# Performance work log

Hardware: AMD Instinct MI355X
Metric: run time of the kernel (lower is better)

Reference implementation:

```python
import jax, jax.numpy as jnp
import numpy as np

B, T, N, D = 8, 512, 64, 128
PRED, HEADS, HID = 96, 8, 256
KERNELS = (17, 49)
NUM_LAYERS = 1
NUM_BLOCKS = 1
IDX_T = np.arange(64)   # lowest 64 of T//2=256 rfft modes (mode_select='low')
IDX_C = np.arange(32)   # min(modes, (N+1)//2)=32 lowest channel-frequency modes


def _mov_avg(x, k):
    # x: [B, T, N]; replicate-pad (k-1)//2 on both ends, then box filter (AvgPool1d stride 1)
    pad = (k - 1) // 2
    xp = jnp.concatenate([jnp.repeat(x[:, :1], pad, axis=1), x, jnp.repeat(x[:, -1:], pad, axis=1)], axis=1)
    c = jnp.cumsum(xp, axis=1)
    c = jnp.concatenate([jnp.zeros_like(c[:, :1]), c], axis=1)
    return (c[:, k:] - c[:, :-k]) / k


def _decomp_multi(x, dec_w, dec_b):
    # series_decomp_multi: softmax-weighted mixture of moving averages
    mm = jnp.stack([_mov_avg(x, k) for k in KERNELS], axis=-1)        # [B,T,N,K]
    w = jax.nn.softmax(x[..., None] * dec_w + dec_b, axis=-1)         # Linear(1,K) on x, softmax over K
    trend = jnp.sum(mm * w, axis=-1)
    return x - trend, trend


def _complex_attn(x, Wq, Wk, Wv, Wo):
    # x: complex64 [B, L, M, D]; multi-head attention over the M selected frequency modes.
    # Real projection weights applied to complex activations; attention weights are
    # softmax over |q k^H| / sqrt(dh); values stay complex.
    Bq, L, M, Dm = x.shape
    dh = Dm // HEADS
    q = jnp.einsum('blmd,de->blme', x, Wq).reshape(Bq, L, M, HEADS, dh)
    k = jnp.einsum('blmd,de->blme', x, Wk).reshape(Bq, L, M, HEADS, dh)
    v = jnp.einsum('blmd,de->blme', x, Wv).reshape(Bq, L, M, HEADS, dh)
    s = jnp.einsum('blmhd,blnhd->blhmn', q, jnp.conj(k))              # complex scores
    w = jax.nn.softmax(jnp.abs(s) / np.sqrt(dh), axis=-1)             # real attn weights
    o = jnp.einsum('blhmn,blnhd->blmhd', w.astype(x.dtype), v).reshape(Bq, L, M, Dm)
    return jnp.einsum('blmd,de->blme', o, Wo)


def _cem(x, Wq, Wk, Wv, Wo):
    # channel-frequency attention; x: [B, N, T, D]
    xp = jnp.transpose(x, (0, 2, 1, 3))                               # [B,T,N,D]
    xf = jnp.fft.rfft(xp, axis=2)                                     # [B,T,N//2+1,D]
    xs = xf[:, :, IDX_C, :]                                           # gather selected modes
    for _ in range(NUM_LAYERS):
        xs = _complex_attn(xs, Wq, Wk, Wv, Wo)
    yf = jnp.zeros((x.shape[0], T, N // 2 + 1, D), dtype=xf.dtype).at[:, :, IDX_C, :].set(xs)
    y = jnp.fft.irfft(yf, n=N, axis=2)
    return jnp.transpose(y, (0, 2, 1, 3))


def _tem(x, Wq, Wk, Wv, Wo):
    # temporal-frequency attention; x: [B, N, T, D]
    xf = jnp.fft.rfft(x, axis=2)                                      # [B,N,T//2+1,D]
    xs = xf[:, :, IDX_T, :]
    for _ in range(NUM_LAYERS):
        xs = _complex_attn(xs, Wq, Wk, Wv, Wo)
    yf = jnp.zeros((x.shape[0], N, T // 2 + 1, D), dtype=xf.dtype).at[:, :, IDX_T, :].set(xs)
    return jnp.fft.irfft(yf, n=T, axis=2)


def setup_inputs() -> dict:
    key = jax.random.key(0)
    ks = jax.random.split(key, 24)
    r = lambda i, shape, s: jax.random.normal(ks[i], shape, jnp.float32) * s
    K = len(KERNELS)
    return {
        'x': jax.random.normal(ks[0], (B, T, N), jnp.float32),
        'embeddings': jax.random.normal(ks[1], (1, D), jnp.float32),
        'dec_w': r(2, (K,), 1.0),
        'dec_b': jnp.zeros((K,), jnp.float32),
        'mlp_w1': r(3, (T, HID), 1.0 / np.sqrt(T)),
        'mlp_b1': jnp.zeros((HID,), jnp.float32),
        'mlp_w2': r(4, (HID, HID), 1.0 / np.sqrt(HID)),
        'mlp_b2': jnp.zeros((HID,), jnp.float32),
        'mlp_w3': r(5, (HID, PRED), 1.0 / np.sqrt(HID)),
        'mlp_b3': jnp.zeros((PRED,), jnp.float32),
        'cem_Wq': r(6, (D, D), 0.02), 'cem_Wk': r(7, (D, D), 0.02),
        'cem_Wv': r(8, (D, D), 0.02), 'cem_Wo': r(9, (D, D), 0.02),
        'tem_Wq': r(10, (D, D), 0.02), 'tem_Wk': r(11, (D, D), 0.02),
        'tem_Wv': r(12, (D, D), 0.02), 'tem_Wo': r(13, (D, D), 0.02),
        'dr_w': r(14, (D, 1), 1.0 / np.sqrt(D)),
        'dr_b': jnp.zeros((1,), jnp.float32),
        'out_w': r(15, (T, PRED), 1.0 / np.sqrt(T)),
        'out_b': jnp.zeros((PRED,), jnp.float32),
        'W_fuse': jnp.ones((2,), jnp.float32),
    }


def reference(x, embeddings, dec_w, dec_b, mlp_w1, mlp_b1, mlp_w2, mlp_b2, mlp_w3, mlp_b3,
              cem_Wq, cem_Wk, cem_Wv, cem_Wo, tem_Wq, tem_Wk, tem_Wv, tem_Wo,
              dr_w, dr_b, out_w, out_b, W_fuse):
    res, trend = _decomp_multi(x, dec_w, dec_b)
    t = jnp.transpose(trend, (0, 2, 1))                               # [B,N,T]
    h = jax.nn.relu(t @ mlp_w1 + mlp_b1)
    h = jax.nn.relu(h @ mlp_w2 + mlp_b2)
    trend_out = jnp.transpose(h @ mlp_w3 + mlp_b3, (0, 2, 1))         # [B,PRED,N]
    # tokenEmb: [B,T,N] -> [B,N,T,1] * [1,D]
    xe = jnp.transpose(res, (0, 2, 1))[..., None] * embeddings[0]      # [B,N,T,D]
    for _ in range(NUM_BLOCKS):
        xe = _cem(xe, cem_Wq, cem_Wk, cem_Wv, cem_Wo)
    for _ in range(NUM_BLOCKS):
        xe = _tem(xe, tem_Wq, tem_Wk, tem_Wv, tem_Wo)
    xr = jnp.einsum('bntd,do->bnto', xe, dr_w)[..., 0] + dr_b[0]      # dim_reduction -> [B,N,T]
    xo = jnp.transpose(jnp.einsum('bnt,tp->bnp', xr, out_w) + out_b, (0, 2, 1))  # [B,PRED,N]
    return W_fuse[0] * xo + W_fuse[1] * trend_out
```

## Files before the change

### kernel.cpp

```cpp
#include <hip/hip_runtime.h>
#include <hip/hip_bf16.h>

typedef __hip_bfloat16 bf16;
typedef float v2f __attribute__((ext_vector_type(2)));

constexpr int CB = 8;
constexpr int CT = 512;
constexpr int CN = 64;
constexpr int CD = 128;
constexpr int CP = 96;
constexpr int CH = 8;
constexpr int CDH = 16;
constexpr int CHID = 256;
constexpr int CM = 32;
constexpr int CG = 64;
constexpr float TWO_PI = 6.28318530717958647692f;

__device__ __forceinline__ float LD(const void* p, size_t i, bool f) {
  return f ? ((const float*)p)[i] : __bfloat162float(((const bf16*)p)[i]);
}
template <bool F32>
__device__ __forceinline__ float LDT(const void* p, size_t i) {
  return F32 ? ((const float*)p)[i] : __bfloat162float(((const bf16*)p)[i]);
}

__device__ __forceinline__ bool detect_f32(const void* x) {
  const unsigned int* xw = (const unsigned int*)x;
  unsigned int w = xw[threadIdx.x & 63];
  unsigned int e = (w >> 7) & 0xFF;
  unsigned long long m = __ballot(e >= 0x90 || e <= 0x60);
  return __popcll(m) > 3;
}

struct MArgs {
  const void *x, *dec_w, *dec_b, *out_w, *emb, *cWq, *cWk, *cWv, *cWo;
  const void *tWq, *tWk, *tWv, *tWo, *drw, *drb, *out_b, *wfuse;
  const void *w1, *b1, *w2, *b2, *w3, *b3;
  float *trendo, *Pbuf, *ewq, *ewk, *ewv, *wod, *owr, *owi;
  void* out;
};

template <bool F32>
__device__ void k2_body(float* sm, const MArgs& a) {
  float* xbuf = sm;
  float* rows = sm;
  float* h1 = sm + 1536;
  float* h2 = sm + 2048;
  int r0 = blockIdx.x * 2;
  int b = r0 >> 6, n0 = r0 & 63;
  int tid = threadIdx.x;
  size_t xb = (size_t)b * CT * CN + n0;
  for (int i = tid; i < CT * 2; i += 256) {
    int t = i >> 1, q = i & 1;
    xbuf[t * 3 + q] = LDT<F32>(a.x, xb + (size_t)t * CN + q);
  }
  __syncthreads();
  float trv[4];
  int q = tid & 1, tl = tid >> 1, t0 = tl * 4;
  {
    float w0 = LDT<F32>(a.dec_w, 0), w1 = LDT<F32>(a.dec_w, 1);
    float c0 = LDT<F32>(a.dec_b, 0), c1 = LDT<F32>(a.dec_b, 1);
    float s17 = 0.f, s49 = 0.f;
    #pragma unroll
    for (int o = -8; o <= 8; ++o) {
      int u = t0 + o; u = u < 0 ? 0 : (u > CT - 1 ? CT - 1 : u);
      s17 += xbuf[u * 3 + q];
    }
    #pragma unroll
    for (int o = -24; o <= 24; ++o) {
      int u = t0 + o; u = u < 0 ? 0 : (u > CT - 1 ? CT - 1 : u);
      s49 += xbuf[u * 3 + q];
    }
    #pragma unroll
    for (int k = 0; k < 4; ++k) {
      int t = t0 + k;
      if (k > 0) {
        int up8 = t + 8 > CT - 1 ? CT - 1 : t + 8;
        int dn9 = t - 9 < 0 ? 0 : t - 9;
        int up24 = t + 24 > CT - 1 ? CT - 1 : t + 24;
        int dn25 = t - 25 < 0 ? 0 : t - 25;
        s17 += xbuf[up8 * 3 + q] - xbuf[dn9 * 3 + q];
        s49 += xbuf[up24 * 3 + q] - xbuf[dn25 * 3 + q];
      }
      float m0 = s17 * (1.f / 17.f), m1 = s49 * (1.f / 49.f);
      float xv = xbuf[t * 3 + q];
      float l0 = xv * w0 + c0, l1 = xv * w1 + c1;
      float mx = fmaxf(l0, l1);
      float e0 = __expf(l0 - mx), e1 = __expf(l1 - mx);
      trv[k] = (e0 * m0 + e1 * m1) / (e0 + e1);
    }
  }
  __syncthreads();
  #pragma unroll
  for (int k = 0; k < 4; ++k) rows[q * CT + t0 + k] = trv[k];
  __syncthreads();
  int c = tid;
  float a0, a1;
  {
    float bias = LDT<F32>(a.b1, c);
    a0 = a1 = 0.f;
    #pragma unroll 16
    for (int t = 0; t < CT; ++t) {
      float w = LDT<F32>(a.w1, t * CHID + c);
      a0 = fmaf(rows[t], w, a0);
      a1 = fmaf(rows[CT + t], w, a1);
    }
    h1[c] = fmaxf(a0 + bias, 0.f);
    h1[CHID + c] = fmaxf(a1 + bias, 0.f);
  }
  __syncthreads();
  {
    float bias = LDT<F32>(a.b2, c);
    a0 = a1 = 0.f;
    #pragma unroll 16
    for (int i = 0; i < CHID; ++i) {
      float w = LDT<F32>(a.w2, i * CHID + c);
      a0 = fmaf(h1[i], w, a0);
      a1 = fmaf(h1[CHID + i], w, a1);
    }
    h2[c] = fmaxf(a0 + bias, 0.f);
    h2[CHID + c] = fmaxf(a1 + bias, 0.f);
  }
  __syncthreads();
  if (tid < 2 * CP) {
    int p = tid < CP ? tid : tid - CP;
    int qh = tid < CP ? 0 : 1;
    float bias = LDT<F32>(a.b3, p);
    a0 = 0.f;
    #pragma unroll 16
    for (int i = 0; i < CHID; ++i)
      a0 = fmaf(h2[qh * CHID + i], LDT<F32>(a.w3, i * CP + p), a0);
    a.trendo[((size_t)(b * CN + n0 + qh)) * CP + p] = a0 + bias;
  }
}

__global__ __launch_bounds__(256, 4) void kS2(MArgs a) {
  __shared__ __align__(16) float sm[4608];
  bool f32 = detect_f32(a.x);
  int blk = blockIdx.x, tid = threadIdx.x;
  if (blk < 256) {
    if (f32) k2_body<true>(sm, a);
    else     k2_body<false>(sm, a);
  } else if (blk < 1280) {
    float* xl = sm;
    float2* SL = (float2*)sm;
    float* chp = sm + 3328;
    float* rowl = sm + 3328;
    float* Rr = sm + 3584;
    float* Ri = sm + 3712;
    float* aR = sm + 3840;
    float* prod = sm + 3968;
    float* chl = sm + 4096;
    float* eml = sm + 4104;
    int bk = blk - 256;
    int b = bk >> 7, tbase = (bk & 127) * 4;
    int w = tid >> 6, lane = tid & 63;
    size_t xb = (size_t)b * CT * CN;
    for (int i = tid; i < 52 * 64; i += 256) {
      int r = i >> 6, n = i & 63;
      int u = tbase - 24 + r; u = u < 0 ? 0 : (u > CT - 1 ? CT - 1 : u);
      xl[i] = LD(a.x, xb + (size_t)u * CN + n, f32);
    }
    if (tid < 128) eml[tid] = LD(a.emb, tid, f32);
    __syncthreads();
    {
      const void* Wm = (w < 2) ? a.cWq : a.cWk;
      int d0 = (w & 1) * 64;
      float p0 = 0.f, p1 = 0.f;
      #pragma unroll 16
      for (int d = d0; d < d0 + 64; ++d) {
        float em = eml[d];
        p0 = fmaf(em, LD(Wm, (size_t)d * CD + lane, f32), p0);
        p1 = fmaf(em, LD(Wm, (size_t)d * CD + 64 + lane, f32), p1);
      }
      chp[w * 128 + lane] = p0;
      chp[w * 128 + 64 + lane] = p1;
    }
    __syncthreads();
    if (tid < 128) {
      float pq = chp[tid] + chp[128 + tid];
      float pk = chp[256 + tid] + chp[384 + tid];
      prod[tid] = pq * pk;
    }
    __syncthreads();
    if (tid < CH) {
      float s = 0;
      #pragma unroll
      for (int j = 0; j < 16; ++j) s += prod[tid * 16 + j];
      chl[tid] = fabsf(s);
    }
    {
      int Lt = 24 + w;
      float w0 = LD(a.dec_w, 0, f32), w1 = LD(a.dec_w, 1, f32);
      float c0 = LD(a.dec_b, 0, f32), c1 = LD(a.dec_b, 1, f32);
      const float* xc = xl + Lt * 64 + lane;
      float pa = 0.f, pb = 0.f;
      #pragma unroll
      for (int o = -8; o <= 8; o += 2) pa += xc[o * 64];
      #pragma unroll
      for (int o = -7; o <= 7; o += 2) pb += xc[o * 64];
      float s17 = pa + pb;
      float qa = 0.f, qb = 0.f;
      #pragma unroll
      for (int o = 9; o <= 23; o += 2) qa += xc[o * 64] + xc[-o * 64];
      #pragma unroll
      for (int o = 10; o <= 24; o += 2) qb += xc[o * 64] + xc[-o * 64];
      float s49 = s17 + qa + qb;
      float m0 = s17 * (1.f / 17.f), m1 = s49 * (1.f / 49.f);
      float xv = xc[0];
      float l0 = xv * w0 + c0, l1 = xv * w1 + c1;
      float mx = fmaxf(l0, l1);
      float e0 = __expf(l0 - mx), e1 = __expf(l1 - mx);
      float tr = (e0 * m0 + e1 * m1) / (e0 + e1);
      rowl[w * 64 + lane] = xv - tr;
    }
    __syncthreads();
    float am, amax;
    {
      int m = lane & 31, half = lane >> 5;
      float cf, sf;
      sincosf((float)m * (TWO_PI / CN), &sf, &cf);
      float wr = (half & m & 1) ? -1.f : 1.f, wi = 0.f;
      float rr = 0.f, ri = 0.f;
      const float* rw = rowl + w * 64 + half * 32;
      #pragma unroll 8
      for (int j = 0; j < 32; ++j) {
        float xv = rw[j];
        rr = fmaf(xv, wr, rr);
        ri = fmaf(-xv, wi, ri);
        float nr = wr * cf - wi * sf; wi = wi * cf + wr * sf; wr = nr;
      }
      rr += __shfl_xor(rr, 32);
      ri += __shfl_xor(ri, 32);
      am = sqrtf(rr * rr + ri * ri);
      if (half == 0) { Rr[w * 32 + m] = rr; Ri[w * 32 + m] = ri; aR[w * 32 + m] = am; }
      amax = am;
      #pragma unroll
      for (int s2 = 1; s2 < 32; s2 <<= 1) amax = fmaxf(amax, __shfl_xor(amax, s2));
    }
    __syncthreads();
    {
      float base2 = 0.25f * 1.44269504f * am;
      int hb = lane >> 5;
      float al0 = chl[hb] * base2;
      float al1 = chl[hb + 2] * base2;
      float al2 = chl[hb + 4] * base2;
      float al3 = chl[hb + 6] * base2;
      float den0 = 0, sr0 = 0, si0 = 0, den1 = 0, sr1 = 0, si1 = 0;
      float den2 = 0, sr2 = 0, si2 = 0, den3 = 0, sr3 = 0, si3 = 0;
      const float* aRw = aR + w * 32;
      const float* Rrw = Rr + w * 32;
      const float* Riw = Ri + w * 32;
      for (int n2 = 0; n2 < CM; ++n2) {
        float d = aRw[n2] - amax;
        float rrn = Rrw[n2], rin = Riw[n2];
        float e0 = exp2f(al0 * d); den0 += e0; sr0 = fmaf(e0, rrn, sr0); si0 = fmaf(e0, rin, si0);
        float e1 = exp2f(al1 * d); den1 += e1; sr1 = fmaf(e1, rrn, sr1); si1 = fmaf(e1, rin, si1);
        float e2 = exp2f(al2 * d); den2 += e2; sr2 = fmaf(e2, rrn, sr2); si2 = fmaf(e2, rin, si2);
        float e3 = exp2f(al3 * d); den3 += e3; sr3 = fmaf(e3, rrn, sr3); si3 = fmaf(e3, rin, si3);
      }
      float r0 = 1.f / den0, r1 = 1.f / den1, r2 = 1.f / den2, r3 = 1.f / den3;
      SL[w * 256 + lane      ] = make_float2(sr0 * r0, si0 * r0);
      SL[w * 256 + lane + 64 ] = make_float2(sr1 * r1, si1 * r1);
      SL[w * 256 + lane + 128] = make_float2(sr2 * r2, si2 * r2);
      SL[w * 256 + lane + 192] = make_float2(sr3 * r3, si3 * r3);
    }
    __syncthreads();
    {
      int n2 = lane;
      const float2* Sw = SL + w * 256;
      float cd, sd;
      sincosf((float)n2 * (TWO_PI / CN), &sd, &cd);
      float c2 = cd * cd - sd * sd, s2 = 2.f * sd * cd;
      float pxA = 1.f, pyA = 0.f;
      float acc[8];
      #pragma unroll
      for (int h = 0; h < CH; ++h) acc[h] = -Sw[h * 32].x;
      for (int f2 = 0; f2 < 16; ++f2) {
        float pxB = pxA * cd - pyA * sd, pyB = pyA * cd + pxA * sd;
        #pragma unroll
        for (int h = 0; h < CH; ++h) {
          float4 sv = *(const float4*)(Sw + h * 32 + f2 * 2);
          acc[h] += 2.f * (sv.x * pxA - sv.y * pyA) + 2.f * (sv.z * pxB - sv.w * pyB);
        }
        float nx = pxA * c2 - pyA * s2; pyA = pyA * c2 + pxA * s2; pxA = nx;
      }
      int t = tbase + w;
      float* Pb = a.Pbuf + (((size_t)(b * CN + n2)) * CT + t) * CH;
      ((float4*)Pb)[0] = make_float4(acc[0] * (1.f / CN), acc[1] * (1.f / CN),
                                     acc[2] * (1.f / CN), acc[3] * (1.f / CN));
      ((float4*)Pb)[1] = make_float4(acc[4] * (1.f / CN), acc[5] * (1.f / CN),
                                     acc[6] * (1.f / CN), acc[7] * (1.f / CN));
    }
  } else if (blk < 1344) {
    float* ps = sm;
    int g = blk - 1280;
    int tc = tid >> 7, idx = tid & 127;
    if (idx < CP) {
      int p = idx, t0 = tc * 256;
      float s0, c0v, ss, cs;
      sincosf((float)((g * t0) & (CT - 1)) * (TWO_PI / CT), &s0, &c0v);
      sincosf((float)g * (TWO_PI / CT), &ss, &cs);
      float wr = c0v, wi = s0, ar = 0.f, ai = 0.f;
      #pragma unroll 16
      for (int t = 0; t < 256; ++t) {
        float w = LD(a.out_w, (size_t)(t0 + t) * CP + p, f32);
        ar = fmaf(w, wr, ar); ai = fmaf(w, wi, ai);
        float nr = wr * cs - wi * ss; wi = wi * cs + wr * ss; wr = nr;
      }
      ps[(tc * CP + p) * 2] = ar; ps[(tc * CP + p) * 2 + 1] = ai;
    }
    __syncthreads();
    if (tid < CP) {
      a.owr[g * CP + tid] = ps[tid * 2] + ps[(CP + tid) * 2];
      a.owi[g * CP + tid] = ps[tid * 2 + 1] + ps[(CP + tid) * 2 + 1];
    }
  } else if (blk < 1356) {
    float* eml = sm;
    float* evl = sm + 128;
    float* ewoh = sm + 160;
    int bi = blk - 1344;
    int half = tid >> 7, e = tid & 127;
    int pairIdx = bi * 2 + half;
    int which = pairIdx >> 3, h = pairIdx & 7;
    if (tid < 128) eml[tid] = LD(a.emb, tid, f32);
    __syncthreads();
    if (e < 16) {
      float acc = 0;
      #pragma unroll 8
      for (int d = 0; d < CD; ++d) acc += eml[d] * LD(a.cWv, d * CD + h * CDH + e, f32);
      evl[half * 16 + e] = acc;
    }
    __syncthreads();
    {
      float acc = 0;
      #pragma unroll
      for (int j = 0; j < CDH; ++j)
        acc += evl[half * 16 + j] * LD(a.cWo, (h * CDH + j) * CD + e, f32);
      ewoh[half * 128 + e] = acc;
    }
    __syncthreads();
    {
      const void* W = which == 0 ? a.tWq : (which == 1 ? a.tWk : a.tWv);
      float acc = 0;
      #pragma unroll 8
      for (int d = 0; d < CD; ++d) acc += ewoh[half * 128 + d] * LD(W, d * CD + e, f32);
      (which == 0 ? a.ewq : (which == 1 ? a.ewk : a.ewv))[h * CD + e] = acc;
    }
  } else {
    float* drl = sm;
    if (tid < 128) drl[tid] = LD(a.drw, tid, f32);
    __syncthreads();
    if (tid < 128) {
      float acc = 0;
      #pragma unroll 8
      for (int d = 0; d < CD; ++d) acc += LD(a.tWo, tid * CD + d, f32) * drl[d];
      a.wod[tid] = acc;
    }
  }
}

__global__ __launch_bounds__(1024, 2) void kC(MArgs a) {
  __shared__ __align__(16) float sm[8384];
  float* Pl = sm;
  float* QL = sm + 4352;
  float* Cl = sm + 5632;
  float* Ul = sm + 6144;
  float2* vdL = (float2*)(sm + 6208);
  float2* mrg = (float2*)(sm + 6208);
  float2* zL = (float2*)(sm + 7232);
  float* zrow = sm + 8256;
  float4* mrgP = (float4*)sm;
  bool f32 = detect_f32(a.x);
  int blk = blockIdx.x, tid = threadIdx.x;
  int b = blk >> 6, n = blk & 63;
  const float4* src4 = (const float4*)(a.Pbuf + ((size_t)(b * CN + n)) * CT * CH);
  {
    float4 v = src4[tid];
    int t = tid >> 1, half = tid & 1;
    int k = t >> 6, u = t & 63;
    float* dst = Pl + u * 68 + half * 32 + k;
    dst[0] = v.x; dst[8] = v.y; dst[16] = v.z; dst[24] = v.w;
  }
  if (tid < 576) {
    if (tid < 512) {
      int h = tid >> 6, aa = (tid >> 3) & 7, b2 = tid & 7;
      float c = 0;
      #pragma unroll
      for (int j = 0; j < CDH; ++j)
        c += a.ewq[aa * CD + h * CDH + j] * a.ewk[b2 * CD + h * CDH + j];
      Cl[tid] = c;
    } else {
      int r = tid - 512;
      int h = r >> 3, aa = r & 7;
      float c = 0;
      #pragma unroll
      for (int j = 0; j < CDH; ++j) c += a.ewv[aa * CD + h * CDH + j] * a.wod[h * CDH + j];
      Ul[r] = c;
    }
  }
  __syncthreads();
  float p2_qr, p2_qi;
  int p2_uh = tid >> 9, p2_r = tid & 511;
  {
    int g = p2_r >> 3, h = p2_r & 7, uh = p2_uh;
    float cs1, sn1;
    sincosf((float)g * (TWO_PI / CT), &sn1, &cs1);
    float cs = cs1 * cs1 - sn1 * sn1;
    float sn = 2.f * sn1 * cs1;
    float wr = uh ? cs1 : 1.f, wi = uh ? -sn1 : 0.f;
    float car[8] = {0, 0, 0, 0, 0, 0, 0, 0};
    float cai[8] = {0, 0, 0, 0, 0, 0, 0, 0};
    const float* Pbase = Pl + uh * 68 + h * 8;
    #pragma unroll 4
    for (int v = 0; v < 32; ++v) {
      const float4* pu = (const float4*)(Pbase + v * 136);
      float4 lo = pu[0], hi = pu[1];
      car[0] = fmaf(lo.x, wr, car[0]); cai[0] = fmaf(lo.x, wi, cai[0]);
      car[1] = fmaf(lo.y, wr, car[1]); cai[1] = fmaf(lo.y, wi, cai[1]);
      car[2] = fmaf(lo.z, wr, car[2]); cai[2] = fmaf(lo.z, wi, cai[2]);
      car[3] = fmaf(lo.w, wr, car[3]); cai[3] = fmaf(lo.w, wi, cai[3]);
      car[4] = fmaf(hi.x, wr, car[4]); cai[4] = fmaf(hi.x, wi, cai[4]);
      car[5] = fmaf(hi.y, wr, car[5]); cai[5] = fmaf(hi.y, wi, cai[5]);
      car[6] = fmaf(hi.z, wr, car[6]); cai[6] = fmaf(hi.z, wi, cai[6]);
      car[7] = fmaf(hi.w, wr, car[7]); cai[7] = fmaf(hi.w, wi, cai[7]);
      float nr = wr * cs + wi * sn; wi = wi * cs - wr * sn; wr = nr;
    }
    float cs8, sn8;
    sincosf((float)(g & 7) * (TWO_PI / 8.f), &sn8, &cs8);
    float pr = 1.f, pi = 0.f, qr = 0.f, qi = 0.f;
    #pragma unroll
    for (int k = 0; k < 8; ++k) {
      qr += car[k] * pr - cai[k] * pi;
      qi += cai[k] * pr + car[k] * pi;
      float nr2 = pr * cs8 + pi * sn8; pi = pi * cs8 - pr * sn8; pr = nr2;
    }
    p2_qr = qr; p2_qi = qi;
    if (uh == 1) mrg[p2_r] = make_float2(qr, qi);
  }
  __syncthreads();
  if (p2_uh == 0) {
    int g = p2_r >> 3, h = p2_r & 7;
    float2 o = mrg[p2_r];
    QL[g * 20 + h * 2]     = p2_qr + o.x;
    QL[g * 20 + h * 2 + 1] = p2_qi + o.y;
  }
  __syncthreads();
  int gh = tid >> 9, r3 = tid & 511;
  int h = r3 >> 6, m = r3 & 63;
  v2f qp[8];
  {
    const float4* q4 = (const float4*)(QL + m * 20);
    #pragma unroll
    for (int j = 0; j < 4; ++j) {
      float4 qv = q4[j];
      qp[2 * j]     = (v2f){qv.x, qv.y};
      qp[2 * j + 1] = (v2f){qv.z, qv.w};
    }
  }
  if (gh == 0) {
    float vr = 0, vi = 0;
    #pragma unroll
    for (int aa = 0; aa < 8; ++aa) {
      float u = Ul[h * 8 + aa];
      vr = fmaf(qp[aa].x, u, vr); vi = fmaf(qp[aa].y, u, vi);
    }
    vdL[h * 64 + m] = make_float2(vr, vi);
  }
  v2f uu[8], vv[8];
  #pragma unroll
  for (int bb = 0; bb < 8; ++bb) {
    v2f acc = {0.f, 0.f};
    #pragma unroll
    for (int aa = 0; aa < 8; ++aa) acc += qp[aa] * Cl[(h * 8 + aa) * 8 + bb];
    uu[bb] = acc;
    vv[bb] = (v2f){acc.y, -acc.x};
  }
  __syncthreads();
  float mx = -1e30f, den = 0.f, zr = 0.f, zi = 0.f;
  #pragma unroll 4
  for (int gi = 0; gi < 32; ++gi) {
    int g = gh * 32 + gi;
    const float4* y4 = (const float4*)(QL + g * 20);
    v2f sr2 = {0.f, 0.f}, si2 = {0.f, 0.f};
    #pragma unroll
    for (int j = 0; j < 4; ++j) {
      float4 yv = y4[j];
      v2f ya = {yv.x, yv.y}, yb = {yv.z, yv.w};
      sr2 = uu[2 * j] * ya + sr2;
      si2 = vv[2 * j] * ya + si2;
      sr2 = uu[2 * j + 1] * yb + sr2;
      si2 = vv[2 * j + 1] * yb + si2;
    }
    float sr = sr2.x + sr2.y;
    float si = si2.x + si2.y;
    float s = 0.25f * sqrtf(sr * sr + si * si);
    if (s > mx) {
      float f = __expf(mx - s);
      den *= f; zr *= f; zi *= f; mx = s;
    }
    float e = __expf(s - mx);
    float2 vd = vdL[h * 64 + g];
    den += e; zr += e * vd.x; zi += e * vd.y;
  }
  if (gh == 1) mrgP[r3] = make_float4(mx, den, zr, zi);
  __syncthreads();
  if (gh == 0) {
    float4 o = mrgP[r3];
    float M = fmaxf(mx, o.x);
    float ea = __expf(mx - M), eb = __expf(o.x - M);
    den = den * ea + o.y * eb;
    zr = zr * ea + o.z * eb;
    zi = zi * ea + o.w * eb;
    float rv = 1.f / den;
    zL[h * 64 + m] = make_float2(zr * rv, zi * rv);
  }
  __syncthreads();
  if (tid < 128) {
    int g = tid >> 1, c = tid & 1;
    float acc = 0;
    #pragma unroll
    for (int hh = 0; hh < CH; ++hh) acc += c ? zL[hh * 64 + g].y : zL[hh * 64 + g].x;
    zrow[g * 2 + c] = acc;
  }
  __syncthreads();
  if (tid < CP) {
    int p = tid;
    float acc = zrow[0] * a.owr[p] - zrow[1] * a.owi[p];
    #pragma unroll 8
    for (int g = 1; g < CG; ++g)
      acc += 2.f * (zrow[g * 2] * a.owr[g * CP + p] - zrow[g * 2 + 1] * a.owi[g * CP + p]);
    float xo = acc * (1.f / CT) + LD(a.drb, 0, f32) * a.owr[p] + LD(a.out_b, p, f32);
    float val = LD(a.wfuse, 0, f32) * xo
              + LD(a.wfuse, 1, f32) * a.trendo[((size_t)(b * CN + n)) * CP + p];
    size_t oidx = ((size_t)(b * CP + p)) * CN + n;
    if (f32) ((float*)a.out)[oidx] = val;
    else ((bf16*)a.out)[oidx] = __float2bfloat16(val);
  }
}

extern "C" void kernel_launch(void* const* d_in, const int* in_sizes, int n_in,
                              void* d_out, int out_size, void* d_ws, size_t ws_size,
                              hipStream_t stream) {
  float* W = (float*)d_ws;
  MArgs a;
  a.x = d_in[0];   a.emb = d_in[1];  a.dec_w = d_in[2]; a.dec_b = d_in[3];
  a.w1 = d_in[4];  a.b1 = d_in[5];   a.w2 = d_in[6];    a.b2 = d_in[7];
  a.w3 = d_in[8];  a.b3 = d_in[9];
  a.cWq = d_in[10]; a.cWk = d_in[11]; a.cWv = d_in[12]; a.cWo = d_in[13];
  a.tWq = d_in[14]; a.tWk = d_in[15]; a.tWv = d_in[16]; a.tWo = d_in[17];
  a.drw = d_in[18]; a.drb = d_in[19]; a.out_w = d_in[20]; a.out_b = d_in[21];
  a.wfuse = d_in[22];
  a.trendo = W; W += (size_t)CB * CN * CP;
  a.Pbuf = W;   W += (size_t)CB * CN * CT * CH;
  a.ewq = W;    W += CH * CD;
  a.ewk = W;    W += CH * CD;
  a.ewv = W;    W += CH * CD;
  a.wod = W;    W += CD;
  a.owr = W;    W += CG * CP;
  a.owi = W;    W += CG * CP;
  a.out = d_out;

  kS2<<<1357, 256, 0, stream>>>(a);
  kC<<<512, 1024, 0, stream>>>(a);
}
```

Measured before the change: 187.4 us.

## Vectorize trend MLP weight loads with split-K partials; halve attention block threads

```diff
diff --git a/kernel.cpp b/kernel.cpp
--- a/kernel.cpp
+++ b/kernel.cpp
@@ -2,7 +2,6 @@
 #include <hip/hip_bf16.h>
 
 typedef __hip_bfloat16 bf16;
-typedef float v2f __attribute__((ext_vector_type(2)));
 
 constexpr int CB = 8;
 constexpr int CT = 512;
@@ -23,6 +22,12 @@
 __device__ __forceinline__ float LDT(const void* p, size_t i) {
   return F32 ? ((const float*)p)[i] : __bfloat162float(((const bf16*)p)[i]);
 }
+__device__ __forceinline__ float b2f(short s) {
+  return __uint_as_float(((unsigned int)(unsigned short)s) << 16);
+}
+__device__ __forceinline__ float rdlane(float v, int l) {
+  return __int_as_float(__builtin_amdgcn_readlane(__float_as_int(v), l));
+}
 
 __device__ __forceinline__ bool detect_f32(const void* x) {
   const unsigned int* xw = (const unsigned int*)x;
@@ -46,6 +51,7 @@
   float* rows = sm;
   float* h1 = sm + 1536;
   float* h2 = sm + 2048;
+  float* part = sm + 2560;
   int r0 = blockIdx.x * 2;
   int b = r0 >> 6, n0 = r0 & 63;
   int tid = threadIdx.x;
@@ -94,39 +100,94 @@
   #pragma unroll
   for (int k = 0; k < 4; ++k) rows[q * CT + t0 + k] = trv[k];
   __syncthreads();
-  int c = tid;
-  float a0, a1;
-  {
+  int tt = tid >> 6, cq = tid & 63;
+  {
+    float ac0 = 0, ac1 = 0, ac2 = 0, ac3 = 0, ac4 = 0, ac5 = 0, ac6 = 0, ac7 = 0;
+    int tg = tt * 128;
+    if (F32) {
+      const float4* w4 = (const float4*)a.w1;
+      #pragma unroll 8
+      for (int t = tg; t < tg + 128; ++t) {
+        float4 wv = w4[t * 64 + cq];
+        float rA = rows[t], rB = rows[CT + t];
+        ac0 = fmaf(rA, wv.x, ac0); ac1 = fmaf(rA, wv.y, ac1);
+        ac2 = fmaf(rA, wv.z, ac2); ac3 = fmaf(rA, wv.w, ac3);
+        ac4 = fmaf(rB, wv.x, ac4); ac5 = fmaf(rB, wv.y, ac5);
+        ac6 = fmaf(rB, wv.z, ac6); ac7 = fmaf(rB, wv.w, ac7);
+      }
+    } else {
+      const short4* w4 = (const short4*)a.w1;
+      #pragma unroll 8
+      for (int t = tg; t < tg + 128; ++t) {
+        short4 sv = w4[t * 64 + cq];
+        float wx = b2f(sv.x), wy = b2f(sv.y), wz = b2f(sv.z), ww = b2f(sv.w);
+        float rA = rows[t], rB = rows[CT + t];
+        ac0 = fmaf(rA, wx, ac0); ac1 = fmaf(rA, wy, ac1);
+        ac2 = fmaf(rA, wz, ac2); ac3 = fmaf(rA, ww, ac3);
+        ac4 = fmaf(rB, wx, ac4); ac5 = fmaf(rB, wy, ac5);
+        ac6 = fmaf(rB, wz, ac6); ac7 = fmaf(rB, ww, ac7);
+      }
+    }
+    float4* pp = (float4*)(part + tt * 512 + cq * 4);
+    pp[0] = make_float4(ac0, ac1, ac2, ac3);
+    pp[64] = make_float4(ac4, ac5, ac6, ac7);
+  }
+  __syncthreads();
+  {
+    int c = tid;
     float bias = LDT<F32>(a.b1, c);
-    a0 = a1 = 0.f;
-    #pragma unroll 16
-    for (int t = 0; t < CT; ++t) {
-      float w = LDT<F32>(a.w1, t * CHID + c);
-      a0 = fmaf(rows[t], w, a0);
-      a1 = fmaf(rows[CT + t], w, a1);
-    }
-    h1[c] = fmaxf(a0 + bias, 0.f);
-    h1[CHID + c] = fmaxf(a1 + bias, 0.f);
-  }
-  __syncthreads();
-  {
+    float s0 = part[c] + part[512 + c] + part[1024 + c] + part[1536 + c];
+    float s1 = part[256 + c] + part[768 + c] + part[1280 + c] + part[1792 + c];
+    h1[c] = fmaxf(s0 + bias, 0.f);
+    h1[CHID + c] = fmaxf(s1 + bias, 0.f);
+  }
+  __syncthreads();
+  {
+    float ac0 = 0, ac1 = 0, ac2 = 0, ac3 = 0, ac4 = 0, ac5 = 0, ac6 = 0, ac7 = 0;
+    int ig = tt * 64;
+    if (F32) {
+      const float4* w4 = (const float4*)a.w2;
+      #pragma unroll 8
+      for (int i = ig; i < ig + 64; ++i) {
+        float4 wv = w4[i * 64 + cq];
+        float rA = h1[i], rB = h1[CHID + i];
+        ac0 = fmaf(rA, wv.x, ac0); ac1 = fmaf(rA, wv.y, ac1);
+        ac2 = fmaf(rA, wv.z, ac2); ac3 = fmaf(rA, wv.w, ac3);
+        ac4 = fmaf(rB, wv.x, ac4); ac5 = fmaf(rB, wv.y, ac5);
+        ac6 = fmaf(rB, wv.z, ac6); ac7 = fmaf(rB, wv.w, ac7);
+      }
+    } else {
+      const short4* w4 = (const short4*)a.w2;
+      #pragma unroll 8
+      for (int i = ig; i < ig + 64; ++i) {
+        short4 sv = w4[i * 64 + cq];
+        float wx = b2f(sv.x), wy = b2f(sv.y), wz = b2f(sv.z), ww = b2f(sv.w);
+        float rA = h1[i], rB = h1[CHID + i];
+        ac0 = fmaf(rA, wx, ac0); ac1 = fmaf(rA, wy, ac1);
+        ac2 = fmaf(rA, wz, ac2); ac3 = fmaf(rA, ww, ac3);
+        ac4 = fmaf(rB, wx, ac4); ac5 = fmaf(rB, wy, ac5);
+        ac6 = fmaf(rB, wz, ac6); ac7 = fmaf(rB, ww, ac7);
+      }
+    }
+    float4* pp = (float4*)(part + tt * 512 + cq * 4);
+    pp[0] = make_float4(ac0, ac1, ac2, ac3);
+    pp[64] = make_float4(ac4, ac5, ac6, ac7);
+  }
+  __syncthreads();
+  {
+    int c = tid;
     float bias = LDT<F32>(a.b2, c);
-    a0 = a1 = 0.f;
-    #pragma unroll 16
-    for (int i = 0; i < CHID; ++i) {
-      float w = LDT<F32>(a.w2, i * CHID + c);
-      a0 = fmaf(h1[i], w, a0);
-      a1 = fmaf(h1[CHID + i], w, a1);
-    }
-    h2[c] = fmaxf(a0 + bias, 0.f);
-    h2[CHID + c] = fmaxf(a1 + bias, 0.f);
+    float s0 = part[c] + part[512 + c] + part[1024 + c] + part[1536 + c];
+    float s1 = part[256 + c] + part[768 + c] + part[1280 + c] + part[1792 + c];
+    h2[c] = fmaxf(s0 + bias, 0.f);
+    h2[CHID + c] = fmaxf(s1 + bias, 0.f);
   }
   __syncthreads();
   if (tid < 2 * CP) {
     int p = tid < CP ? tid : tid - CP;
     int qh = tid < CP ? 0 : 1;
     float bias = LDT<F32>(a.b3, p);
-    a0 = 0.f;
+    float a0 = 0.f;
     #pragma unroll 16
     for (int i = 0; i < CHID; ++i)
       a0 = fmaf(h2[qh * CHID + i], LDT<F32>(a.w3, i * CP + p), a0);
@@ -360,38 +421,36 @@
   }
 }
 
-__global__ __launch_bounds__(1024, 2) void kC(MArgs a) {
+__global__ __launch_bounds__(512, 4) void kC(MArgs a) {
   __shared__ __align__(16) float sm[8384];
   float* Pl = sm;
   float* QL = sm + 4352;
   float* Cl = sm + 5632;
   float* Ul = sm + 6144;
   float2* vdL = (float2*)(sm + 6208);
-  float2* mrg = (float2*)(sm + 6208);
   float2* zL = (float2*)(sm + 7232);
   float* zrow = sm + 8256;
-  float4* mrgP = (float4*)sm;
   bool f32 = detect_f32(a.x);
   int blk = blockIdx.x, tid = threadIdx.x;
   int b = blk >> 6, n = blk & 63;
   const float4* src4 = (const float4*)(a.Pbuf + ((size_t)(b * CN + n)) * CT * CH);
-  {
-    float4 v = src4[tid];
-    int t = tid >> 1, half = tid & 1;
+  for (int i = tid; i < 1024; i += 512) {
+    float4 v = src4[i];
+    int t = i >> 1, half = i & 1;
     int k = t >> 6, u = t & 63;
     float* dst = Pl + u * 68 + half * 32 + k;
     dst[0] = v.x; dst[8] = v.y; dst[16] = v.z; dst[24] = v.w;
   }
-  if (tid < 576) {
-    if (tid < 512) {
-      int h = tid >> 6, aa = (tid >> 3) & 7, b2 = tid & 7;
+  for (int id = tid; id < 512 + 64; id += 512) {
+    if (id < 512) {
+      int h = id >> 6, aa = (id >> 3) & 7, b2 = id & 7;
       float c = 0;
       #pragma unroll
       for (int j = 0; j < CDH; ++j)
         c += a.ewq[aa * CD + h * CDH + j] * a.ewk[b2 * CD + h * CDH + j];
-      Cl[tid] = c;
+      Cl[id] = c;
     } else {
-      int r = tid - 512;
+      int r = id - 512;
       int h = r >> 3, aa = r & 7;
       float c = 0;
       #pragma unroll
@@ -400,21 +459,16 @@
     }
   }
   __syncthreads();
-  float p2_qr, p2_qi;
-  int p2_uh = tid >> 9, p2_r = tid & 511;
-  {
-    int g = p2_r >> 3, h = p2_r & 7, uh = p2_uh;
-    float cs1, sn1;
-    sincosf((float)g * (TWO_PI / CT), &sn1, &cs1);
-    float cs = cs1 * cs1 - sn1 * sn1;
-    float sn = 2.f * sn1 * cs1;
-    float wr = uh ? cs1 : 1.f, wi = uh ? -sn1 : 0.f;
+  {
+    int g = tid >> 3, h = tid & 7;
+    float cs, sn;
+    sincosf((float)g * (TWO_PI / CT), &sn, &cs);
+    float wr = 1.f, wi = 0.f;
     float car[8] = {0, 0, 0, 0, 0, 0, 0, 0};
     float cai[8] = {0, 0, 0, 0, 0, 0, 0, 0};
-    const float* Pbase = Pl + uh * 68 + h * 8;
     #pragma unroll 4
-    for (int v = 0; v < 32; ++v) {
-      const float4* pu = (const float4*)(Pbase + v * 136);
+    for (int u = 0; u < 64; ++u) {
+      const float4* pu = (const float4*)(Pl + u * 68 + h * 8);
       float4 lo = pu[0], hi = pu[1];
       car[0] = fmaf(lo.x, wr, car[0]); cai[0] = fmaf(lo.x, wi, cai[0]);
       car[1] = fmaf(lo.y, wr, car[1]); cai[1] = fmaf(lo.y, wi, cai[1]);
@@ -435,65 +489,54 @@
       qi += cai[k] * pr + car[k] * pi;
       float nr2 = pr * cs8 + pi * sn8; pi = pi * cs8 - pr * sn8; pr = nr2;
     }
-    p2_qr = qr; p2_qi = qi;
-    if (uh == 1) mrg[p2_r] = make_float2(qr, qi);
-  }
-  __syncthreads();
-  if (p2_uh == 0) {
-    int g = p2_r >> 3, h = p2_r & 7;
-    float2 o = mrg[p2_r];
-    QL[g * 20 + h * 2]     = p2_qr + o.x;
-    QL[g * 20 + h * 2 + 1] = p2_qi + o.y;
-  }
-  __syncthreads();
-  int gh = tid >> 9, r3 = tid & 511;
-  int h = r3 >> 6, m = r3 & 63;
-  v2f qp[8];
+    QL[g * 20 + h * 2] = qr;
+    QL[g * 20 + h * 2 + 1] = qi;
+  }
+  __syncthreads();
+  int h = tid >> 6, m = tid & 63;
+  float qrow[16];
   {
     const float4* q4 = (const float4*)(QL + m * 20);
-    #pragma unroll
-    for (int j = 0; j < 4; ++j) {
-      float4 qv = q4[j];
-      qp[2 * j]     = (v2f){qv.x, qv.y};
-      qp[2 * j + 1] = (v2f){qv.z, qv.w};
-    }
-  }
-  if (gh == 0) {
+    float4 q0 = q4[0], q1 = q4[1], q2 = q4[2], q3 = q4[3];
+    qrow[0] = q0.x; qrow[1] = q0.y; qrow[2] = q0.z; qrow[3] = q0.w;
+    qrow[4] = q1.x; qrow[5] = q1.y; qrow[6] = q1.z; qrow[7] = q1.w;
+    qrow[8] = q2.x; qrow[9] = q2.y; qrow[10] = q2.z; qrow[11] = q2.w;
+    qrow[12] = q3.x; qrow[13] = q3.y; qrow[14] = q3.z; qrow[15] = q3.w;
+  }
+  {
     float vr = 0, vi = 0;
     #pragma unroll
     for (int aa = 0; aa < 8; ++aa) {
       float u = Ul[h * 8 + aa];
-      vr = fmaf(qp[aa].x, u, vr); vi = fmaf(qp[aa].y, u, vi);
+      vr = fmaf(qrow[2 * aa], u, vr); vi = fmaf(qrow[2 * aa + 1], u, vi);
     }
     vdL[h * 64 + m] = make_float2(vr, vi);
   }
-  v2f uu[8], vv[8];
+  float uux[8], uuy[8];
   #pragma unroll
   for (int bb = 0; bb < 8; ++bb) {
-    v2f acc = {0.f, 0.f};
-    #pragma unroll
-    for (int aa = 0; aa < 8; ++aa) acc += qp[aa] * Cl[(h * 8 + aa) * 8 + bb];
-    uu[bb] = acc;
-    vv[bb] = (v2f){acc.y, -acc.x};
-  }
-  __syncthreads();
+    float ax = 0, ay = 0;
+    #pragma unroll
+    for (int aa = 0; aa < 8; ++aa) {
+      float cl = Cl[(h * 8 + aa) * 8 + bb];
+      ax = fmaf(qrow[2 * aa], cl, ax);
+      ay = fmaf(qrow[2 * aa + 1], cl, ay);
+    }
+    uux[bb] = ax; uuy[bb] = ay;
+  }
   float mx = -1e30f, den = 0.f, zr = 0.f, zi = 0.f;
   #pragma unroll 4
-  for (int gi = 0; gi < 32; ++gi) {
-    int g = gh * 32 + gi;
-    const float4* y4 = (const float4*)(QL + g * 20);
-    v2f sr2 = {0.f, 0.f}, si2 = {0.f, 0.f};
-    #pragma unroll
-    for (int j = 0; j < 4; ++j) {
-      float4 yv = y4[j];
-      v2f ya = {yv.x, yv.y}, yb = {yv.z, yv.w};
-      sr2 = uu[2 * j] * ya + sr2;
-      si2 = vv[2 * j] * ya + si2;
-      sr2 = uu[2 * j + 1] * yb + sr2;
-      si2 = vv[2 * j + 1] * yb + si2;
-    }
-    float sr = sr2.x + sr2.y;
-    float si = si2.x + si2.y;
+  for (int g = 0; g < CG; ++g) {
+    float sr = 0.f, si = 0.f;
+    #pragma unroll
+    for (int j = 0; j < 8; ++j) {
+      float ya = rdlane(qrow[2 * j], g);
+      float yb = rdlane(qrow[2 * j + 1], g);
+      sr = fmaf(uux[j], ya, sr);
+      sr = fmaf(uuy[j], yb, sr);
+      si = fmaf(uuy[j], ya, si);
+      si = fmaf(uux[j], -yb, si);
+    }
     float s = 0.25f * sqrtf(sr * sr + si * si);
     if (s > mx) {
       float f = __expf(mx - s);
@@ -501,17 +544,9 @@
     }
     float e = __expf(s - mx);
     float2 vd = vdL[h * 64 + g];
-    den += e; zr += e * vd.x; zi += e * vd.y;
-  }
-  if (gh == 1) mrgP[r3] = make_float4(mx, den, zr, zi);
-  __syncthreads();
-  if (gh == 0) {
-    float4 o = mrgP[r3];
-    float M = fmaxf(mx, o.x);
-    float ea = __expf(mx - M), eb = __expf(o.x - M);
-    den = den * ea + o.y * eb;
-    zr = zr * ea + o.z * eb;
-    zi = zi * ea + o.w * eb;
+    den += e; zr = fmaf(e, vd.x, zr); zi = fmaf(e, vd.y, zi);
+  }
+  {
     float rv = 1.f / den;
     zL[h * 64 + m] = make_float2(zr * rv, zi * rv);
   }
@@ -562,5 +597,5 @@
   a.out = d_out;
 
   kS2<<<1357, 256, 0, stream>>>(a);
-  kC<<<512, 1024, 0, stream>>>(a);
-}
+  kC<<<512, 512, 0, stream>>>(a);
+}
```

New measurement: 198.0 us. +5.6%, slower.

## Factor temporal DFT into radix-8 butterflies and halve kC block size

Applied to the files above, without the earlier changes.

```diff
diff --git a/kernel.cpp b/kernel.cpp
--- a/kernel.cpp
+++ b/kernel.cpp
@@ -360,38 +360,37 @@
   }
 }
 
-__global__ __launch_bounds__(1024, 2) void kC(MArgs a) {
-  __shared__ __align__(16) float sm[8384];
+__global__ __launch_bounds__(512, 4) void kC(MArgs a) {
+  __shared__ __align__(16) float sm[13504];
   float* Pl = sm;
   float* QL = sm + 4352;
   float* Cl = sm + 5632;
   float* Ul = sm + 6144;
   float2* vdL = (float2*)(sm + 6208);
-  float2* mrg = (float2*)(sm + 6208);
   float2* zL = (float2*)(sm + 7232);
   float* zrow = sm + 8256;
-  float4* mrgP = (float4*)sm;
+  float* Ab = sm + 8384;
   bool f32 = detect_f32(a.x);
   int blk = blockIdx.x, tid = threadIdx.x;
   int b = blk >> 6, n = blk & 63;
   const float4* src4 = (const float4*)(a.Pbuf + ((size_t)(b * CN + n)) * CT * CH);
-  {
-    float4 v = src4[tid];
-    int t = tid >> 1, half = tid & 1;
+  for (int i = tid; i < 1024; i += 512) {
+    float4 v = src4[i];
+    int t = i >> 1, half = i & 1;
     int k = t >> 6, u = t & 63;
     float* dst = Pl + u * 68 + half * 32 + k;
     dst[0] = v.x; dst[8] = v.y; dst[16] = v.z; dst[24] = v.w;
   }
-  if (tid < 576) {
-    if (tid < 512) {
-      int h = tid >> 6, aa = (tid >> 3) & 7, b2 = tid & 7;
+  for (int id = tid; id < 512 + 64; id += 512) {
+    if (id < 512) {
+      int h = id >> 6, aa = (id >> 3) & 7, b2 = id & 7;
       float c = 0;
       #pragma unroll
       for (int j = 0; j < CDH; ++j)
         c += a.ewq[aa * CD + h * CDH + j] * a.ewk[b2 * CD + h * CDH + j];
-      Cl[tid] = c;
+      Cl[id] = c;
     } else {
-      int r = tid - 512;
+      int r = id - 512;
       int h = r >> 3, aa = r & 7;
       float c = 0;
       #pragma unroll
@@ -400,54 +399,53 @@
     }
   }
   __syncthreads();
-  float p2_qr, p2_qi;
-  int p2_uh = tid >> 9, p2_r = tid & 511;
-  {
-    int g = p2_r >> 3, h = p2_r & 7, uh = p2_uh;
-    float cs1, sn1;
-    sincosf((float)g * (TWO_PI / CT), &sn1, &cs1);
-    float cs = cs1 * cs1 - sn1 * sn1;
-    float sn = 2.f * sn1 * cs1;
-    float wr = uh ? cs1 : 1.f, wi = uh ? -sn1 : 0.f;
-    float car[8] = {0, 0, 0, 0, 0, 0, 0, 0};
-    float cai[8] = {0, 0, 0, 0, 0, 0, 0, 0};
-    const float* Pbase = Pl + uh * 68 + h * 8;
+  {
+    int u = tid >> 3, h = tid & 7;
+    const float* pr = Pl + u * 68 + h * 8;
+    float p0 = pr[0], p1 = pr[1], p2 = pr[2], p3 = pr[3];
+    float p4 = pr[4], p5 = pr[5], p6 = pr[6], p7 = pr[7];
+    const float s = 0.70710678118654752f;
+    float p04a = p0 + p4, p04s = p0 - p4;
+    float p26a = p2 + p6, p26s = p2 - p6;
+    float p17a = p1 + p7, p17s = p1 - p7;
+    float p35a = p3 + p5, p35s = p3 - p5;
+    float e1 = s * (p17a - p35a);
+    float e2 = s * (p17s + p35s);
+    float* ab = Ab + u * 80 + h * 10;
+    ab[0] = p04a + p26a + p17a + p35a;
+    ab[1] = 0.f;
+    ab[2] = p04s + e1;
+    ab[3] = -e2 - p26s;
+    ab[4] = p04a - p26a;
+    ab[5] = -(p17s - p35s);
+    ab[6] = p04s - e1;
+    ab[7] = -e2 + p26s;
+    ab[8] = (p04a + p26a) - (p17a + p35a);
+    ab[9] = 0.f;
+  }
+  __syncthreads();
+  {
+    int g = tid >> 3, h = tid & 7;
+    int rho = g & 7;
+    int rc = rho < 5 ? rho : 8 - rho;
+    float csgn = rho < 5 ? 1.f : -1.f;
+    float cs, sn;
+    sincosf((float)g * (TWO_PI / CT), &sn, &cs);
+    float wr = 1.f, wi = 0.f, qr = 0.f, qi = 0.f;
+    const float2* ab = (const float2*)(Ab + h * 10 + rc * 2);
     #pragma unroll 4
-    for (int v = 0; v < 32; ++v) {
-      const float4* pu = (const float4*)(Pbase + v * 136);
-      float4 lo = pu[0], hi = pu[1];
-      car[0] = fmaf(lo.x, wr, car[0]); cai[0] = fmaf(lo.x, wi, cai[0]);
-      car[1] = fmaf(lo.y, wr, car[1]); cai[1] = fmaf(lo.y, wi, cai[1]);
-      car[2] = fmaf(lo.z, wr, car[2]); cai[2] = fmaf(lo.z, wi, cai[2]);
-      car[3] = fmaf(lo.w, wr, car[3]); cai[3] = fmaf(lo.w, wi, cai[3]);
-      car[4] = fmaf(hi.x, wr, car[4]); cai[4] = fmaf(hi.x, wi, cai[4]);
-      car[5] = fmaf(hi.y, wr, car[5]); cai[5] = fmaf(hi.y, wi, cai[5]);
-      car[6] = fmaf(hi.z, wr, car[6]); cai[6] = fmaf(hi.z, wi, cai[6]);
-      car[7] = fmaf(hi.w, wr, car[7]); cai[7] = fmaf(hi.w, wi, cai[7]);
+    for (int u = 0; u < 64; ++u) {
+      float2 A = ab[u * 40];
+      float are = A.x, aim = csgn * A.y;
+      qr = fmaf(are, wr, qr); qr = fmaf(-aim, wi, qr);
+      qi = fmaf(are, wi, qi); qi = fmaf(aim, wr, qi);
       float nr = wr * cs + wi * sn; wi = wi * cs - wr * sn; wr = nr;
     }
-    float cs8, sn8;
-    sincosf((float)(g & 7) * (TWO_PI / 8.f), &sn8, &cs8);
-    float pr = 1.f, pi = 0.f, qr = 0.f, qi = 0.f;
-    #pragma unroll
-    for (int k = 0; k < 8; ++k) {
-      qr += car[k] * pr - cai[k] * pi;
-      qi += cai[k] * pr + car[k] * pi;
-      float nr2 = pr * cs8 + pi * sn8; pi = pi * cs8 - pr * sn8; pr = nr2;
-    }
-    p2_qr = qr; p2_qi = qi;
-    if (uh == 1) mrg[p2_r] = make_float2(qr, qi);
-  }
-  __syncthreads();
-  if (p2_uh == 0) {
-    int g = p2_r >> 3, h = p2_r & 7;
-    float2 o = mrg[p2_r];
-    QL[g * 20 + h * 2]     = p2_qr + o.x;
-    QL[g * 20 + h * 2 + 1] = p2_qi + o.y;
-  }
-  __syncthreads();
-  int gh = tid >> 9, r3 = tid & 511;
-  int h = r3 >> 6, m = r3 & 63;
+    QL[g * 20 + h * 2] = qr;
+    QL[g * 20 + h * 2 + 1] = qi;
+  }
+  __syncthreads();
+  int h = tid >> 6, m = tid & 63;
   v2f qp[8];
   {
     const float4* q4 = (const float4*)(QL + m * 20);
@@ -458,7 +456,7 @@
       qp[2 * j + 1] = (v2f){qv.z, qv.w};
     }
   }
-  if (gh == 0) {
+  {
     float vr = 0, vi = 0;
     #pragma unroll
     for (int aa = 0; aa < 8; ++aa) {
@@ -476,11 +474,9 @@
     uu[bb] = acc;
     vv[bb] = (v2f){acc.y, -acc.x};
   }
-  __syncthreads();
   float mx = -1e30f, den = 0.f, zr = 0.f, zi = 0.f;
   #pragma unroll 4
-  for (int gi = 0; gi < 32; ++gi) {
-    int g = gh * 32 + gi;
+  for (int g = 0; g < CG; ++g) {
     const float4* y4 = (const float4*)(QL + g * 20);
     v2f sr2 = {0.f, 0.f}, si2 = {0.f, 0.f};
     #pragma unroll
@@ -501,17 +497,9 @@
     }
     float e = __expf(s - mx);
     float2 vd = vdL[h * 64 + g];
-    den += e; zr += e * vd.x; zi += e * vd.y;
-  }
-  if (gh == 1) mrgP[r3] = make_float4(mx, den, zr, zi);
-  __syncthreads();
-  if (gh == 0) {
-    float4 o = mrgP[r3];
-    float M = fmaxf(mx, o.x);
-    float ea = __expf(mx - M), eb = __expf(o.x - M);
-    den = den * ea + o.y * eb;
-    zr = zr * ea + o.z * eb;
-    zi = zi * ea + o.w * eb;
+    den += e; zr = fmaf(e, vd.x, zr); zi = fmaf(e, vd.y, zi);
+  }
+  {
     float rv = 1.f / den;
     zL[h * 64 + m] = make_float2(zr * rv, zi * rv);
   }
@@ -562,5 +550,5 @@
   a.out = d_out;
 
   kS2<<<1357, 256, 0, stream>>>(a);
-  kC<<<512, 1024, 0, stream>>>(a);
-}
+  kC<<<512, 512, 0, stream>>>(a);
+}
```

Result: faster. 181.7 us (-3.1%).
